# Kernel tuning notes

Hardware: AMD Instinct MI355X
Metric: run time of the kernel (lower is better)

The kernel has to match this reference:

```python
import jax, jax.numpy as jnp
import numpy as np

B, S, D = 1024, 200, 128
NQ, NC, NQD, NCD = 50000, 1000, 101, 101


def _linear_params(k, fan_in, fan_out):
    bound = 1.0 / np.sqrt(fan_in)
    kw, kb = jax.random.split(k)
    W = jax.random.uniform(kw, (fan_out, fan_in), minval=-bound, maxval=bound, dtype=jnp.float32)
    b = jax.random.uniform(kb, (fan_out,), minval=-bound, maxval=bound, dtype=jnp.float32)
    return W, b


def setup_inputs() -> dict:
    key = jax.random.key(0)
    ks = jax.random.split(key, 17)
    Wx, bx = _linear_params(ks[0], 4 * D, D)
    Ws1, bs1 = _linear_params(ks[1], D, D)
    Ws2, bs2 = _linear_params(ks[2], D, D)
    Wp1, bp1 = _linear_params(ks[3], 2 * D, D)
    Wp2, bp2 = _linear_params(ks[4], 2 * D, D)
    Wk, bk = _linear_params(ks[5], 4 * D, D)
    Eq = jax.random.normal(ks[6], (NQ, D), dtype=jnp.float32)
    Ec = jax.random.normal(ks[7], (NC, D), dtype=jnp.float32)
    Eqd = jax.random.normal(ks[8], (NQD, D), dtype=jnp.float32)
    Ecd = jax.random.normal(ks[9], (NCD, D), dtype=jnp.float32)
    Ecorr = jax.random.normal(ks[10], (2, D), dtype=jnp.float32)
    # xavier_uniform init for h_pre (torch: gain*sqrt(6/(fan_in+fan_out)) on [B,D])
    bh = np.sqrt(6.0 / (B + D))
    h0 = jax.random.uniform(ks[11], (B, D), minval=-bh, maxval=bh, dtype=jnp.float32)
    question_seq = jax.random.randint(ks[12], (B, S), 0, NQ)
    concept_seq = jax.random.randint(ks[13], (B, S), 0, NC)
    question_diff_seq = jax.random.randint(ks[14], (B, S), 0, NQD)
    concept_diff_seq = jax.random.randint(ks[15], (B, S), 0, NCD)
    correct_seq = jax.random.randint(ks[16], (B, S), 0, 2)
    return dict(question_seq=question_seq, concept_seq=concept_seq,
                question_diff_seq=question_diff_seq, concept_diff_seq=concept_diff_seq,
                correct_seq=correct_seq,
                Eq=Eq, Ec=Ec, Eqd=Eqd, Ecd=Ecd, Ecorr=Ecorr,
                Wx=Wx, bx=bx, Ws1=Ws1, bs1=bs1, Ws2=Ws2, bs2=bs2,
                Wp1=Wp1, bp1=bp1, Wp2=Wp2, bp2=bp2, Wk=Wk, bk=bk, h0=h0)


def reference(question_seq, concept_seq, question_diff_seq, concept_diff_seq, correct_seq,
              Eq, Ec, Eqd, Ecd, Ecorr,
              Wx, bx, Ws1, bs1, Ws2, bs2, Wp1, bp1, Wp2, bp2, Wk, bk, h0):
    qe = Eq[question_seq]            # [B,S,D]
    ce = Ec[concept_seq]
    qde = Eqd[question_diff_seq]
    cde = Ecd[concept_diff_seq]
    corr = Ecorr[correct_seq]
    # generate_x_MLP applied to all timesteps at once (same math as per-step)
    x = jnp.concatenate([qe, ce, qde, cde], axis=-1) @ Wx.T + bx  # [B,S,D]
    # time-major inputs for the scan over t = 0 .. S-2
    xs = (jnp.swapaxes(x[:, :-1], 0, 1),      # x_t       [S-1,B,D]
          jnp.swapaxes(x[:, 1:], 0, 1),       # x_{t+1}
          jnp.swapaxes(corr[:, :-1], 0, 1),
          jnp.swapaxes(qde[:, :-1], 0, 1),
          jnp.swapaxes(cde[:, :-1], 0, 1))

    def step(h_pre, inp):
        xt, xnext, ct, qdt, cdt = inp
        s_in = xt - h_pre
        sdf = jax.nn.sigmoid(s_in @ Ws1.T + bs1) * jnp.tanh(s_in @ Ws2.T + bs2)  # dropout=eval identity
        p_in = jnp.concatenate([sdf, ct], axis=-1)
        pka = jax.nn.sigmoid(p_in @ Wp1.T + bp1) * jnp.tanh(p_in @ Wp2.T + bp2)
        k_in = jnp.concatenate([h_pre, ct, qdt, cdt], axis=-1)
        g = jax.nn.sigmoid(k_in @ Wk.T + bk)
        h = g * h_pre + (1.0 - g) * pka
        yt = jax.nn.sigmoid(jnp.sum(xnext * h, axis=-1))  # [B]
        return h, yt

    _, ys = jax.lax.scan(step, h0, xs)  # ys: [S-1,B]
    y = jnp.concatenate([ys.T, jnp.zeros((question_seq.shape[0], 1), x.dtype)], axis=1)  # [B,S], y[:, S-1]=0
    return y
```

## Files before the change

### kernel.cpp

```cpp
#include <hip/hip_runtime.h>
#include <hip/hip_bf16.h>


#define S_LEN 200
#define NBATCH 1024
#define DIM 128
#define LOG2E 1.4426950408889634f

typedef short short8 __attribute__((ext_vector_type(8)));
typedef float f32x4 __attribute__((ext_vector_type(4)));

__device__ __forceinline__ unsigned short f2b(float f) {
  union { float f; unsigned u; } v; v.f = f;
  unsigned r = (v.u + 0x7FFFu + ((v.u >> 16) & 1u)) >> 16;
  return (unsigned short)r;
}
__device__ __forceinline__ float b2f(unsigned short b) {
  union { unsigned u; float f; } v; v.u = ((unsigned)b) << 16;
  return v.f;
}
__device__ __forceinline__ unsigned pk_bf16(float lo, float hi) {
  __hip_bfloat162 t = __float22bfloat162_rn(make_float2(lo, hi));
  union { __hip_bfloat162 h; unsigned u; } cv; cv.h = t;
  return cv.u;
}
__device__ __forceinline__ float fast_sigmoid(float x) {
  return __builtin_amdgcn_rcpf(1.0f + __builtin_amdgcn_exp2f(-LOG2E * x));
}
__device__ __forceinline__ float fast_tanh(float x) {
  return 2.0f * __builtin_amdgcn_rcpf(1.0f + __builtin_amdgcn_exp2f(-2.0f * LOG2E * x)) - 1.0f;
}
__device__ __forceinline__ void wg_barrier_lds() {
  __asm__ volatile("s_waitcnt lgkmcnt(0)\n\ts_barrier" ::: "memory");
}

__global__ void proj_all_kernel(const float* __restrict__ Eq, const float* __restrict__ Ec,
                                const float* __restrict__ Eqd, const float* __restrict__ Ecd,
                                const float* __restrict__ Ecorr,
                                const float* __restrict__ Wx,
                                const float* __restrict__ Wp1, const float* __restrict__ bp1,
                                const float* __restrict__ Wp2, const float* __restrict__ bp2,
                                const float* __restrict__ Wk, const float* __restrict__ bk,
                                unsigned short* __restrict__ Tq, unsigned short* __restrict__ Tc,
                                unsigned short* __restrict__ Tqd, unsigned short* __restrict__ Tcd,
                                unsigned short* __restrict__ Tkqd, unsigned short* __restrict__ Tkcd,
                                float* __restrict__ Tkc, float* __restrict__ Tp1c,
                                float* __restrict__ Tp2c) {
  const int bid = blockIdx.x;
  const int tid = threadIdx.x;
  if (bid >= 802) {
    const int blk = bid - 802;
    if (blk < 101) {
      const int o = tid & 127, half = tid >> 7;
      const float* e = (half ? Ecd : Eqd) + (size_t)blk * DIM;
      const float* wr = Wk + (size_t)o * 512 + (half ? 384 : 256);
      float a = 0.f;
      for (int k = 0; k < DIM; ++k) a = fmaf(e[k], wr[k], a);
      (half ? Tkcd : Tkqd)[blk * DIM + o] = f2b(a);
    } else {
      for (int idx = tid; idx < 768; idx += 256) {
        const int t = idx >> 8, e = (idx >> 7) & 1, o = idx & 127;
        const float* ec = Ecorr + e * DIM;
        const float* wr; float bias; float* dst;
        if (t == 0)      { wr = Wp1 + (size_t)o * 256 + 128; bias = bp1[o]; dst = Tp1c; }
        else if (t == 1) { wr = Wp2 + (size_t)o * 256 + 128; bias = bp2[o]; dst = Tp2c; }
        else             { wr = Wk  + (size_t)o * 512 + 128; bias = bk[o];  dst = Tkc;  }
        float a = bias;
        for (int k = 0; k < DIM; ++k) a = fmaf(ec[k], wr[k], a);
        dst[e * DIM + o] = a;
      }
    }
    return;
  }
  const float* E; int M, coff, r0; unsigned short* T;
  if (bid < 782)      { E = Eq;  M = 50000; coff = 0;   T = Tq;  r0 = bid * 64; }
  else if (bid < 798) { E = Ec;  M = 1000;  coff = 128; T = Tc;  r0 = (bid - 782) * 64; }
  else if (bid < 800) { E = Eqd; M = 101;   coff = 256; T = Tqd; r0 = (bid - 798) * 64; }
  else                { E = Ecd; M = 101;   coff = 384; T = Tcd; r0 = (bid - 800) * 64; }

  __shared__ __align__(16) unsigned short A[64][136];
  {
    const int row = tid >> 2, cb = (tid & 3) * 32;
    union U8 { uint4 v; unsigned short s[8]; } o;
#pragma unroll
    for (int cc = 0; cc < 4; ++cc) {
      const int c8 = cb + cc * 8;
      if (r0 + row < M) {
        const float4 e0 = *(const float4*)(E + (size_t)(r0 + row) * DIM + c8);
        const float4 e1 = *(const float4*)(E + (size_t)(r0 + row) * DIM + c8 + 4);
        o.s[0] = f2b(e0.x); o.s[1] = f2b(e0.y); o.s[2] = f2b(e0.z); o.s[3] = f2b(e0.w);
        o.s[4] = f2b(e1.x); o.s[5] = f2b(e1.y); o.s[6] = f2b(e1.z); o.s[7] = f2b(e1.w);
      } else {
        o.v = make_uint4(0, 0, 0, 0);
      }
      *(uint4*)&A[row][c8] = o.v;
    }
  }
  __syncthreads();
  const int w = tid >> 6, L = tid & 63, q = L >> 4, m = L & 15;
  short8 bf[2][4];
#pragma unroll
  for (int T2 = 0; T2 < 2; ++T2) {
    const int n = 32 * w + 16 * T2 + m;
#pragma unroll
    for (int kb = 0; kb < 4; ++kb) {
      const float* src = Wx + (size_t)n * 512 + coff + kb * 32 + q * 8;
      const float4 v0 = *(const float4*)src;
      const float4 v1 = *(const float4*)(src + 4);
      short8 f;
      f[0] = (short)f2b(v0.x); f[1] = (short)f2b(v0.y);
      f[2] = (short)f2b(v0.z); f[3] = (short)f2b(v0.w);
      f[4] = (short)f2b(v1.x); f[5] = (short)f2b(v1.y);
      f[6] = (short)f2b(v1.z); f[7] = (short)f2b(v1.w);
      bf[T2][kb] = f;
    }
  }
  const f32x4 vzero = {0.f, 0.f, 0.f, 0.f};
#pragma unroll
  for (int mt = 0; mt < 4; ++mt) {
    short8 af[4];
#pragma unroll
    for (int kb = 0; kb < 4; ++kb) af[kb] = *(const short8*)&A[mt * 16 + m][kb * 32 + q * 8];
    f32x4 acc[2] = {vzero, vzero};
#pragma unroll
    for (int kb = 0; kb < 4; ++kb) {
#pragma unroll
      for (int T2 = 0; T2 < 2; ++T2)
        acc[T2] = __builtin_amdgcn_mfma_f32_16x16x32_bf16(af[kb], bf[T2][kb], acc[T2], 0, 0, 0);
    }
#pragma unroll
    for (int T2 = 0; T2 < 2; ++T2) {
      const int col = 32 * w + 16 * T2 + m;
#pragma unroll
      for (int i = 0; i < 4; ++i) {
        const int r = r0 + mt * 16 + q * 4 + i;
        if (r < M) T[(size_t)r * DIM + col] = f2b(acc[T2][i]);
      }
    }
  }
}

__global__ void build_x_kernel(const int* __restrict__ qs, const int* __restrict__ cs,
                               const int* __restrict__ qds, const int* __restrict__ cds,
                               const int* __restrict__ corr,
                               const unsigned short* __restrict__ Tq, const unsigned short* __restrict__ Tc,
                               const unsigned short* __restrict__ Tqd, const unsigned short* __restrict__ Tcd,
                               const float* __restrict__ bx, unsigned short* __restrict__ xg,
                               float* __restrict__ SSg, float* __restrict__ corrf) {
  const int r = blockIdx.x * 16 + (threadIdx.x >> 4);
  const int c8 = (threadIdx.x & 15) * 8;
  const int s = r >> 10, b = r & 1023;
  const int q = qs[b * S_LEN + s], c = cs[b * S_LEN + s];
  const int qd = qds[b * S_LEN + s], cd = cds[b * S_LEN + s];
  union U8 { uint4 v; unsigned short s[8]; };
  U8 vq, vc, vd, ve, o;
  vq.v = *(const uint4*)(Tq + (size_t)q * DIM + c8);
  vc.v = *(const uint4*)(Tc + (size_t)c * DIM + c8);
  vd.v = *(const uint4*)(Tqd + (size_t)qd * DIM + c8);
  ve.v = *(const uint4*)(Tcd + (size_t)cd * DIM + c8);
  const float4 bx0 = *(const float4*)(bx + c8);
  const float4 bx1 = *(const float4*)(bx + c8 + 4);
  float bb[8] = {bx0.x, bx0.y, bx0.z, bx0.w, bx1.x, bx1.y, bx1.z, bx1.w};
  float part = 0.f;
#pragma unroll
  for (int j = 0; j < 8; ++j) {
    const float sv = b2f(vq.s[j]) + b2f(vc.s[j]) + b2f(vd.s[j]) + b2f(ve.s[j]) + bb[j];
    o.s[j] = f2b(sv);
    const float xr = b2f(o.s[j]);
    part = fmaf(xr, xr, part);
  }
  *(uint4*)(xg + (size_t)r * DIM + c8) = o.v;
#pragma unroll
  for (int off = 1; off <= 8; off <<= 1) part += __shfl_xor(part, off, 64);
  if ((threadIdx.x & 15) == 0) {
    SSg[r] = part;
    corrf[r] = (float)corr[b * S_LEN + s];
  }
}

__global__ void gemm_xg_kernel(const unsigned short* __restrict__ xg,
                               const float* __restrict__ Wk,
                               const int* __restrict__ corr, const int* __restrict__ qds,
                               const int* __restrict__ cds,
                               const float* __restrict__ Tkc,
                               const unsigned short* __restrict__ Tkqd,
                               const unsigned short* __restrict__ Tkcd,
                               unsigned short* __restrict__ GG) {
  const int tid = threadIdx.x;
  const int r0 = blockIdx.x * 64;
  __shared__ __align__(16) unsigned short TS[64][136];
  {
    const int row = tid >> 2, cb = (tid & 3) * 32;
    const int r = r0 + row, t = r >> 10, b = r & 1023;
    const int ci = corr[b * S_LEN + t], qi = qds[b * S_LEN + t], di = cds[b * S_LEN + t];
    union U8 { uint4 v; unsigned short s[8]; };
#pragma unroll
    for (int cc = 0; cc < 4; ++cc) {
      const int c8 = cb + cc * 8;
      U8 vq, vc, o;
      vq.v = *(const uint4*)(Tkqd + (size_t)qi * DIM + c8);
      vc.v = *(const uint4*)(Tkcd + (size_t)di * DIM + c8);
      const float4 k0 = *(const float4*)(Tkc + (size_t)ci * DIM + c8);
      const float4 k1 = *(const float4*)(Tkc + (size_t)ci * DIM + c8 + 4);
      float kk[8] = {k0.x, k0.y, k0.z, k0.w, k1.x, k1.y, k1.z, k1.w};
#pragma unroll
      for (int j = 0; j < 8; ++j) o.s[j] = f2b(kk[j] + b2f(vq.s[j]) + b2f(vc.s[j]));
      *(uint4*)&TS[row][c8] = o.v;
    }
  }
  __syncthreads();
  const int w = tid >> 6, L = tid & 63, q = L >> 4, m = L & 15;
  short8 wk[2][4];
#pragma unroll
  for (int T = 0; T < 2; ++T) {
    const int n = 32 * w + 16 * T + m;
#pragma unroll
    for (int kb = 0; kb < 4; ++kb) {
      const float* src = Wk + (size_t)n * 512 + kb * 32 + q * 8;
      const float4 v0 = *(const float4*)src;
      const float4 v1 = *(const float4*)(src + 4);
      short8 f;
      f[0] = (short)f2b(v0.x); f[1] = (short)f2b(v0.y);
      f[2] = (short)f2b(v0.z); f[3] = (short)f2b(v0.w);
      f[4] = (short)f2b(v1.x); f[5] = (short)f2b(v1.y);
      f[6] = (short)f2b(v1.z); f[7] = (short)f2b(v1.w);
      wk[T][kb] = f;
    }
  }
  const f32x4 vzero = {0.f, 0.f, 0.f, 0.f};
#pragma unroll
  for (int mt = 0; mt < 4; ++mt) {
    short8 af[4];
#pragma unroll
    for (int kb = 0; kb < 4; ++kb)
      af[kb] = *(const short8*)(xg + (size_t)(r0 + mt * 16 + m) * DIM + kb * 32 + q * 8);
    f32x4 acc[2] = {vzero, vzero};
#pragma unroll
    for (int kb = 0; kb < 4; ++kb) {
#pragma unroll
      for (int T = 0; T < 2; ++T)
        acc[T] = __builtin_amdgcn_mfma_f32_16x16x32_bf16(af[kb], wk[T][kb], acc[T], 0, 0, 0);
    }
#pragma unroll
    for (int T = 0; T < 2; ++T) {
      const int col = 32 * w + 16 * T + m;
#pragma unroll
      for (int i = 0; i < 4; ++i) {
        const int row64 = mt * 16 + q * 4 + i;
        GG[(size_t)(r0 + row64) * DIM + col] = f2b(acc[T][i] + b2f(TS[row64][col]));
      }
    }
  }
}

__global__ __launch_bounds__(512, 2) void scan_kernel(
    const unsigned short* __restrict__ xg,
    const unsigned short* __restrict__ gg,
    const float* __restrict__ SSg,
    const float* __restrict__ corrf,
    const float* __restrict__ h0,
    const float* __restrict__ Ws1, const float* __restrict__ bs1,
    const float* __restrict__ Ws2, const float* __restrict__ bs2,
    const float* __restrict__ Wp1, const float* __restrict__ Wp2,
    const float* __restrict__ Wk,
    const float* __restrict__ gTp1c, const float* __restrict__ gTp2c,
    float* __restrict__ outp) {
  __shared__ __align__(16) unsigned short Sbuf[16][136];
  __shared__ __align__(16) unsigned short Pbuf[16][136];

  const int tid = threadIdx.x;
  const int w = tid >> 6, L = tid & 63, q = L >> 4, m = L & 15;
  const int col16 = 16 * w + m;
  const int rbase = blockIdx.x << 4;
  const size_t SB = (size_t)NBATCH * DIM;

  short8 wf[5][4];
  {
    const float* Wptr[5] = {Ws1, Ws2, Wp1, Wp2, Wk};
    const int ldw[5] = {128, 128, 256, 256, 512};
#pragma unroll
    for (int M = 0; M < 5; ++M) {
#pragma unroll
      for (int kb = 0; kb < 4; ++kb) {
        const float* src = Wptr[M] + (size_t)col16 * ldw[M] + kb * 32 + q * 8;
        const float4 v0 = *(const float4*)src;
        const float4 v1 = *(const float4*)(src + 4);
        short8 f;
        f[0] = (short)f2b(v0.x); f[1] = (short)f2b(v0.y);
        f[2] = (short)f2b(v0.z); f[3] = (short)f2b(v0.w);
        f[4] = (short)f2b(v1.x); f[5] = (short)f2b(v1.y);
        f[6] = (short)f2b(v1.z); f[7] = (short)f2b(v1.w);
        wf[M][kb] = f;
      }
    }
  }
  const float bs1v = bs1[col16], bs2v = bs2[col16];
  const float tp1v0 = gTp1c[col16], dtp1 = gTp1c[DIM + col16] - tp1v0;
  const float tp2v0 = gTp2c[col16], dtp2 = gTp2c[DIM + col16] - tp2v0;

  float h[4];
#pragma unroll
  for (int i = 0; i < 4; ++i) {
    const int b = rbase + q * 4 + i;
    const float hv = h0[(size_t)b * DIM + col16];
    h[i] = hv;
    const float xt = b2f(xg[(size_t)b * DIM + col16]);
    Sbuf[q * 4 + i][col16] = f2b(xt - hv);
  }
  if (tid < 16) outp[(size_t)(rbase + tid) * S_LEN + (S_LEN - 1)] = 0.0f;
  float* poy = outp + (size_t)(rbase + m) * S_LEN;

  unsigned short XPA[4], XPB[4], GPA[4], GPB[4];
  float4 CFA, CFB;
  short8 XFA[4], XFB[4];
  float SSA, SSB;
  const unsigned short* pxA = xg + 3 * SB + (size_t)(rbase + q * 4) * DIM + col16;
  const unsigned short* pxB = pxA + SB;
  const unsigned short* pgA = gg + 2 * SB + (size_t)(rbase + q * 4) * DIM + col16;
  const unsigned short* pgB = pgA + SB;
  const float* pcA = corrf + 2 * NBATCH + rbase + q * 4;
  const float* pcB = pcA + NBATCH;
  const unsigned short* pfA = xg + 2 * SB + (size_t)(rbase + m) * DIM + q * 8;
  const unsigned short* pfB = pfA + SB;
  const float* psA = SSg + 2 * NBATCH + rbase + m;
  const float* psB = psA + NBATCH;
#pragma unroll
  for (int i = 0; i < 4; ++i) {
    XPA[i] = xg[SB + (size_t)(rbase + q * 4 + i) * DIM + col16];
    XPB[i] = xg[2 * SB + (size_t)(rbase + q * 4 + i) * DIM + col16];
    GPA[i] = gg[(size_t)(rbase + q * 4 + i) * DIM + col16];
    GPB[i] = gg[SB + (size_t)(rbase + q * 4 + i) * DIM + col16];
  }
  CFA = *(const float4*)(corrf + rbase + q * 4);
  CFB = *(const float4*)(corrf + NBATCH + rbase + q * 4);
#pragma unroll
  for (int kb = 0; kb < 4; ++kb) {
    XFA[kb] = *(const short8*)(xg + (size_t)(rbase + m) * DIM + kb * 32 + q * 8);
    XFB[kb] = *(const short8*)(xg + SB + (size_t)(rbase + m) * DIM + kb * 32 + q * 8);
  }
  SSA = SSg[rbase + m];
  SSB = SSg[NBATCH + rbase + m];

  const f32x4 vzero = {0.f, 0.f, 0.f, 0.f};

#define STEP(TCUR, XP, GP, CF, PX, PG, PC, XF, SSR, PF, PS)                    \
  do {                                                                         \
    const int t_ = (TCUR);                                                     \
    float xnv[4], ggv[4], cfv[4];                                              \
    _Pragma("unroll") for (int i = 0; i < 4; ++i) {                            \
      xnv[i] = b2f(XP[i]); ggv[i] = b2f(GP[i]);                                \
    }                                                                          \
    cfv[0] = CF.x; cfv[1] = CF.y; cfv[2] = CF.z; cfv[3] = CF.w;                \
    short8 xfr[4]; float ssv = SSR;                                            \
    if (w == 0) {                                                              \
      _Pragma("unroll") for (int kb = 0; kb < 4; ++kb) xfr[kb] = XF[kb];       \
    }                                                                          \
    _Pragma("unroll") for (int i = 0; i < 4; ++i) {                            \
      XP[i] = PX[i * DIM]; GP[i] = PG[i * DIM];                                \
    }                                                                          \
    CF = *(const float4*)PC;                                                   \
    PX += 2 * SB; PG += 2 * SB; PC += 2 * NBATCH;                              \
    if (w == 0) {                                                              \
      _Pragma("unroll") for (int kb = 0; kb < 4; ++kb)                         \
        XF[kb] = *(const short8*)(PF + kb * 32);                               \
      SSR = *PS;                                                               \
      PF += 2 * SB; PS += 2 * NBATCH;                                          \
    }                                                                          \
    wg_barrier_lds();                                       \
    short8 sf[4];                                                              \
    _Pragma("unroll") for (int kb = 0; kb < 4; ++kb)                           \
        sf[kb] = *(const short8*)&Sbuf[m][kb * 32 + q * 8];                    \
    f32x4 a1 = vzero, a2 = vzero, c1 = vzero;                                  \
    _Pragma("unroll") for (int kb = 0; kb < 4; ++kb) {                         \
      a1 = __builtin_amdgcn_mfma_f32_16x16x32_bf16(sf[kb], wf[0][kb], a1, 0, 0, 0); \
      a2 = __builtin_amdgcn_mfma_f32_16x16x32_bf16(sf[kb], wf[1][kb], a2, 0, 0, 0); \
      c1 = __builtin_amdgcn_mfma_f32_16x16x32_bf16(sf[kb], wf[4][kb], c1, 0, 0, 0); \
    }                                                                          \
    if (w == 0) {                                                              \
      f32x4 dt = vzero;                                                        \
      _Pragma("unroll") for (int kb = 0; kb < 4; ++kb)                         \
        dt = __builtin_amdgcn_mfma_f32_16x16x32_bf16(sf[kb], xfr[kb], dt, 0, 0, 0); \
      if (t_ > 0 && q == (m >> 2)) {                                           \
        const int ii = m & 3;                                                  \
        const float D = ii == 0 ? dt[0] : ii == 1 ? dt[1] : ii == 2 ? dt[2] : dt[3]; \
        poy[t_ - 1] = fast_sigmoid(ssv - D);                                   \
      }                                                                        \
    }                                                                          \
    _Pragma("unroll") for (int i2 = 0; i2 < 2; ++i2) {                         \
      const float s0 = fast_sigmoid(a1[2 * i2] + bs1v) * fast_tanh(a2[2 * i2] + bs2v); \
      const float s1 = fast_sigmoid(a1[2 * i2 + 1] + bs1v) * fast_tanh(a2[2 * i2 + 1] + bs2v); \
      const unsigned u = pk_bf16(s0, s1);                                      \
      Pbuf[q * 4 + 2 * i2][col16] = (unsigned short)u;                         \
      Pbuf[q * 4 + 2 * i2 + 1][col16] = (unsigned short)(u >> 16);             \
    }                                                                          \
    wg_barrier_lds();                                          \
    short8 pf[4];                                                              \
    _Pragma("unroll") for (int kb = 0; kb < 4; ++kb)                           \
        pf[kb] = *(const short8*)&Pbuf[m][kb * 32 + q * 8];                    \
    f32x4 p1 = vzero, p2 = vzero;                                              \
    _Pragma("unroll") for (int kb = 0; kb < 4; ++kb) {                         \
      p1 = __builtin_amdgcn_mfma_f32_16x16x32_bf16(pf[kb], wf[2][kb], p1, 0, 0, 0); \
      p2 = __builtin_amdgcn_mfma_f32_16x16x32_bf16(pf[kb], wf[3][kb], p2, 0, 0, 0); \
    }                                                                          \
    float sn[4];                                                               \
    _Pragma("unroll") for (int i = 0; i < 4; ++i) {                            \
      const float g = fast_sigmoid(ggv[i] - c1[i]);                            \
      const float t1v = fmaf(cfv[i], dtp1, tp1v0);                             \
      const float t2v = fmaf(cfv[i], dtp2, tp2v0);                             \
      const float pka = fast_sigmoid(p1[i] + t1v) * fast_tanh(p2[i] + t2v);    \
      const float hn = pka + g * (h[i] - pka);                                 \
      h[i] = hn;                                                               \
      sn[i] = xnv[i] - hn;                                                     \
    }                                                                          \
    _Pragma("unroll") for (int i2 = 0; i2 < 2; ++i2) {                         \
      const unsigned u = pk_bf16(sn[2 * i2], sn[2 * i2 + 1]);                  \
      Sbuf[q * 4 + 2 * i2][col16] = (unsigned short)u;                         \
      Sbuf[q * 4 + 2 * i2 + 1][col16] = (unsigned short)(u >> 16);             \
    }                                                                          \
  } while (0)

  for (int t2 = 0; t2 < 198; t2 += 2) {
    STEP(t2, XPA, GPA, CFA, pxA, pgA, pcA, XFA, SSA, pfA, psA);
    STEP(t2 + 1, XPB, GPB, CFB, pxB, pgB, pcB, XFB, SSB, pfB, psB);
  }
  STEP(198, XPA, GPA, CFA, pxA, pgA, pcA, XFA, SSA, pfA, psA);
#undef STEP

  wg_barrier_lds();
  if (w == 0) {
    short8 sf[4];
#pragma unroll
    for (int kb = 0; kb < 4; ++kb) sf[kb] = *(const short8*)&Sbuf[m][kb * 32 + q * 8];
    f32x4 dt = vzero;
#pragma unroll
    for (int kb = 0; kb < 4; ++kb)
      dt = __builtin_amdgcn_mfma_f32_16x16x32_bf16(sf[kb], XFB[kb], dt, 0, 0, 0);
    if (q == (m >> 2)) {
      const int ii = m & 3;
      const float D = ii == 0 ? dt[0] : ii == 1 ? dt[1] : ii == 2 ? dt[2] : dt[3];
      poy[S_LEN - 2] = fast_sigmoid(SSB - D);
    }
  }
}

extern "C" void kernel_launch(void* const* d_in, const int* in_sizes, int n_in,
                              void* d_out, int out_size, void* d_ws, size_t ws_size,
                              hipStream_t stream) {
  const int* qs    = (const int*)d_in[0];
  const int* cs    = (const int*)d_in[1];
  const int* qds   = (const int*)d_in[2];
  const int* cds   = (const int*)d_in[3];
  const int* corr  = (const int*)d_in[4];
  const float* Eq    = (const float*)d_in[5];
  const float* Ec    = (const float*)d_in[6];
  const float* Eqd   = (const float*)d_in[7];
  const float* Ecd   = (const float*)d_in[8];
  const float* Ecorr = (const float*)d_in[9];
  const float* Wx  = (const float*)d_in[10];
  const float* bx  = (const float*)d_in[11];
  const float* Ws1 = (const float*)d_in[12];
  const float* bs1 = (const float*)d_in[13];
  const float* Ws2 = (const float*)d_in[14];
  const float* bs2 = (const float*)d_in[15];
  const float* Wp1 = (const float*)d_in[16];
  const float* bp1 = (const float*)d_in[17];
  const float* Wp2 = (const float*)d_in[18];
  const float* bp2 = (const float*)d_in[19];
  const float* Wk  = (const float*)d_in[20];
  const float* bk  = (const float*)d_in[21];
  const float* h0  = (const float*)d_in[22];

  char* ws = (char*)d_ws;
  const size_t xbytes = (size_t)S_LEN * NBATCH * DIM * 2;
  const size_t A = (xbytes + 255) & ~(size_t)255;
  const size_t ggbytes = (size_t)(S_LEN - 1) * NBATCH * DIM * 2;
  unsigned short* X  = (unsigned short*)ws;
  unsigned short* GG = (unsigned short*)(ws + A);
  unsigned short* Tq  = GG;
  unsigned short* Tc  = (unsigned short*)(ws + A + (size_t)50000 * DIM * 2);
  unsigned short* Tqd = (unsigned short*)(ws + A + (size_t)51000 * DIM * 2);
  unsigned short* Tcd = (unsigned short*)(ws + A + (size_t)51101 * DIM * 2);
  size_t off = A + ((ggbytes + 255) & ~(size_t)255);
  auto alloc = [&](size_t bytes) {
    void* p = ws + off;
    off = (off + bytes + 255) & ~(size_t)255;
    return p;
  };
  float* corrf = (float*)alloc((size_t)S_LEN * NBATCH * 4);
  float* SS    = (float*)alloc((size_t)S_LEN * NBATCH * 4);
  unsigned short* Tkqd = (unsigned short*)alloc((size_t)101 * DIM * 2);
  unsigned short* Tkcd = (unsigned short*)alloc((size_t)101 * DIM * 2);
  float* Tkc  = (float*)alloc((size_t)2 * DIM * 4);
  float* Tp1c = (float*)alloc((size_t)2 * DIM * 4);
  float* Tp2c = (float*)alloc((size_t)2 * DIM * 4);

  proj_all_kernel<<<904, 256, 0, stream>>>(Eq, Ec, Eqd, Ecd, Ecorr, Wx,
                                           Wp1, bp1, Wp2, bp2, Wk, bk,
                                           Tq, Tc, Tqd, Tcd, Tkqd, Tkcd, Tkc, Tp1c, Tp2c);
  build_x_kernel<<<(S_LEN * NBATCH) / 16, 256, 0, stream>>>(qs, cs, qds, cds, corr,
                                                            Tq, Tc, Tqd, Tcd, bx, X, SS, corrf);
  gemm_xg_kernel<<<((S_LEN - 1) * NBATCH) / 64, 256, 0, stream>>>(X, Wk, corr, qds, cds,
                                                                  Tkc, Tkqd, Tkcd, GG);
  scan_kernel<<<64, 512, 0, stream>>>(X, GG, SS, corrf, h0, Ws1, bs1, Ws2, bs2,
                                      Wp1, Wp2, Wk, Tp1c, Tp2c, (float*)d_out);
}
```

Measured before the change: 515.5 us.

## Fuse input build and gate GEMM into scan kernel as producer blocks with watermark sync

Replaces the separate build_x and gemm_xg launches with a single persistent kernel. In it, 64 blocks run the recurrent scan while 191 producer blocks build X, SS, corr and the gate pre-activations per timestep chunk. A coordinator block turns per-timestep completion counters into a watermark that scan blocks poll before each step pair, so input production overlaps the serial scan. It relies on all 256 blocks being co-resident and adds atomic polling overhead. It also gives the workspace a non-aliased layout, falling back to the old path if the workspace is too small.

```diff
diff --git a/kernel.cpp b/kernel.cpp
--- a/kernel.cpp
+++ b/kernel.cpp
@@ -6,6 +6,7 @@
 #define NBATCH 1024
 #define DIM 128
 #define LOG2E 1.4426950408889634f
+#define NPROD 191
 
 typedef short short8 __attribute__((ext_vector_type(8)));
 typedef float f32x4 __attribute__((ext_vector_type(4)));
@@ -45,7 +46,7 @@
                                 unsigned short* __restrict__ Tqd, unsigned short* __restrict__ Tcd,
                                 unsigned short* __restrict__ Tkqd, unsigned short* __restrict__ Tkcd,
                                 float* __restrict__ Tkc, float* __restrict__ Tp1c,
-                                float* __restrict__ Tp2c) {
+                                float* __restrict__ Tp2c, int* __restrict__ syncz) {
   const int bid = blockIdx.x;
   const int tid = threadIdx.x;
   if (bid >= 802) {
@@ -69,6 +70,7 @@
         for (int k = 0; k < DIM; ++k) a = fmaf(ec[k], wr[k], a);
         dst[e * DIM + o] = a;
       }
+      for (int i2 = tid; i2 < 272; i2 += 256) syncz[i2] = 0;
     }
     return;
   }
@@ -253,20 +255,129 @@
   }
 }
 
-__global__ __launch_bounds__(512, 2) void scan_kernel(
-    const unsigned short* __restrict__ xg,
-    const unsigned short* __restrict__ gg,
-    const float* __restrict__ SSg,
-    const float* __restrict__ corrf,
+__device__ __forceinline__ void producer_body(
+    const int p,
+    const int* __restrict__ qs, const int* __restrict__ cs,
+    const int* __restrict__ qds, const int* __restrict__ cds,
+    const int* __restrict__ corr,
+    const unsigned short* __restrict__ Tq, const unsigned short* __restrict__ Tc,
+    const unsigned short* __restrict__ Tqd, const unsigned short* __restrict__ Tcd,
+    const float* __restrict__ bx, const float* __restrict__ Wk,
+    const float* __restrict__ Tkc, const unsigned short* __restrict__ Tkqd,
+    const unsigned short* __restrict__ Tkcd,
+    unsigned short* __restrict__ X, unsigned short* __restrict__ GG,
+    float* __restrict__ SSg, float* __restrict__ corrf,
+    int* donecnt, unsigned short (*xtile)[136], unsigned short (*TS)[136]) {
+  const int tid = threadIdx.x;
+  const int w = tid >> 6, L = tid & 63, q = L >> 4, m = L & 15;
+  const int n = 16 * w + m;
+  short8 wk[4];
+#pragma unroll
+  for (int kb = 0; kb < 4; ++kb) {
+    const float* src = Wk + (size_t)n * 512 + kb * 32 + q * 8;
+    const float4 v0 = *(const float4*)src;
+    const float4 v1 = *(const float4*)(src + 4);
+    short8 f;
+    f[0] = (short)f2b(v0.x); f[1] = (short)f2b(v0.y);
+    f[2] = (short)f2b(v0.z); f[3] = (short)f2b(v0.w);
+    f[4] = (short)f2b(v1.x); f[5] = (short)f2b(v1.y);
+    f[6] = (short)f2b(v1.z); f[7] = (short)f2b(v1.w);
+    wk[kb] = f;
+  }
+  const int row = tid >> 3, k8 = tid & 7;
+  const int c0 = k8 * 16;
+  float bxv[16];
+#pragma unroll
+  for (int j = 0; j < 4; ++j) {
+    const float4 bv = *(const float4*)(bx + c0 + j * 4);
+    bxv[4 * j + 0] = bv.x; bxv[4 * j + 1] = bv.y;
+    bxv[4 * j + 2] = bv.z; bxv[4 * j + 3] = bv.w;
+  }
+  const f32x4 vzero = {0.f, 0.f, 0.f, 0.f};
+  union U8 { uint4 v; unsigned short s[8]; };
+
+  for (int i = p; i < 3200; i += NPROD) {
+    const int t = i >> 4, c = i & 15;
+    const int b = c * 64 + row;
+    const int base = b * S_LEN + t;
+    const int qi = qs[base], ci = cs[base], qdi = qds[base], cdi = cds[base], cri = corr[base];
+    float part = 0.f;
+#pragma unroll
+    for (int jj = 0; jj < 2; ++jj) {
+      const int c8 = c0 + jj * 8;
+      U8 vq, vc, vd, ve, o;
+      vq.v = *(const uint4*)(Tq + (size_t)qi * DIM + c8);
+      vc.v = *(const uint4*)(Tc + (size_t)ci * DIM + c8);
+      vd.v = *(const uint4*)(Tqd + (size_t)qdi * DIM + c8);
+      ve.v = *(const uint4*)(Tcd + (size_t)cdi * DIM + c8);
+#pragma unroll
+      for (int j = 0; j < 8; ++j) {
+        const float sv = b2f(vq.s[j]) + b2f(vc.s[j]) + b2f(vd.s[j]) + b2f(ve.s[j]) + bxv[jj * 8 + j];
+        o.s[j] = f2b(sv);
+        const float xr = b2f(o.s[j]);
+        part = fmaf(xr, xr, part);
+      }
+      *(uint4*)&xtile[row][c8] = o.v;
+      *(uint4*)(X + (size_t)(t * 1024 + b) * DIM + c8) = o.v;
+    }
+#pragma unroll
+    for (int off2 = 1; off2 <= 4; off2 <<= 1) part += __shfl_xor(part, off2, 64);
+    if (k8 == 0) {
+      SSg[t * 1024 + b] = part;
+      corrf[t * 1024 + b] = (float)cri;
+    }
+    if (t < 199) {
+#pragma unroll
+      for (int jj = 0; jj < 2; ++jj) {
+        const int c8 = c0 + jj * 8;
+        U8 vq, vc, o;
+        vq.v = *(const uint4*)(Tkqd + (size_t)qdi * DIM + c8);
+        vc.v = *(const uint4*)(Tkcd + (size_t)cdi * DIM + c8);
+        const float4 k0 = *(const float4*)(Tkc + (size_t)cri * DIM + c8);
+        const float4 k1 = *(const float4*)(Tkc + (size_t)cri * DIM + c8 + 4);
+        float kk[8] = {k0.x, k0.y, k0.z, k0.w, k1.x, k1.y, k1.z, k1.w};
+#pragma unroll
+        for (int j = 0; j < 8; ++j) o.s[j] = f2b(kk[j] + b2f(vq.s[j]) + b2f(vc.s[j]));
+        *(uint4*)&TS[row][c8] = o.v;
+      }
+    }
+    __syncthreads();
+    if (t < 199) {
+#pragma unroll
+      for (int mt = 0; mt < 4; ++mt) {
+        short8 af[4];
+#pragma unroll
+        for (int kb = 0; kb < 4; ++kb) af[kb] = *(const short8*)&xtile[mt * 16 + m][kb * 32 + q * 8];
+        f32x4 acc = vzero;
+#pragma unroll
+        for (int kb = 0; kb < 4; ++kb)
+          acc = __builtin_amdgcn_mfma_f32_16x16x32_bf16(af[kb], wk[kb], acc, 0, 0, 0);
+#pragma unroll
+        for (int i2 = 0; i2 < 4; ++i2) {
+          const int row64 = mt * 16 + q * 4 + i2;
+          GG[(size_t)(t * 1024 + c * 64 + row64) * DIM + n] = f2b(acc[i2] + b2f(TS[row64][n]));
+        }
+      }
+    }
+    __syncthreads();
+    if (tid == 0)
+      __hip_atomic_fetch_add(donecnt + t, 1, __ATOMIC_RELEASE, __HIP_MEMORY_SCOPE_AGENT);
+  }
+}
+
+template <bool PIPE>
+__device__ __forceinline__ void scan_body(
+    const unsigned short* __restrict__ xg, const unsigned short* __restrict__ gg,
+    const float* __restrict__ SSg, const float* __restrict__ corrf,
     const float* __restrict__ h0,
     const float* __restrict__ Ws1, const float* __restrict__ bs1,
     const float* __restrict__ Ws2, const float* __restrict__ bs2,
     const float* __restrict__ Wp1, const float* __restrict__ Wp2,
     const float* __restrict__ Wk,
     const float* __restrict__ gTp1c, const float* __restrict__ gTp2c,
-    float* __restrict__ outp) {
-  __shared__ __align__(16) unsigned short Sbuf[16][136];
-  __shared__ __align__(16) unsigned short Pbuf[16][136];
+    float* __restrict__ outp, int* wmp, unsigned short* ldsbase) {
+  unsigned short (*Sbuf)[136] = (unsigned short (*)[136])ldsbase;
+  unsigned short (*Pbuf)[136] = (unsigned short (*)[136])(ldsbase + 16 * 136);
 
   const int tid = threadIdx.x;
   const int w = tid >> 6, L = tid & 63, q = L >> 4, m = L & 15;
@@ -297,6 +408,16 @@
   const float bs1v = bs1[col16], bs2v = bs2[col16];
   const float tp1v0 = gTp1c[col16], dtp1 = gTp1c[DIM + col16] - tp1v0;
   const float tp2v0 = gTp2c[col16], dtp2 = gTp2c[DIM + col16] - tp2v0;
+  if (tid < 16) outp[(size_t)(rbase + tid) * S_LEN + (S_LEN - 1)] = 0.0f;
+
+  int wm_seen = 0;
+  auto wait_wm = [&](int need) {
+    if (wm_seen >= need) return;
+    while (__hip_atomic_load(wmp, __ATOMIC_RELAXED, __HIP_MEMORY_SCOPE_AGENT) < need)
+      __builtin_amdgcn_s_sleep(8);
+    wm_seen = __hip_atomic_load(wmp, __ATOMIC_ACQUIRE, __HIP_MEMORY_SCOPE_AGENT);
+  };
+  if (PIPE) wait_wm(3);
 
   float h[4];
 #pragma unroll
@@ -307,7 +428,6 @@
     const float xt = b2f(xg[(size_t)b * DIM + col16]);
     Sbuf[q * 4 + i][col16] = f2b(xt - hv);
   }
-  if (tid < 16) outp[(size_t)(rbase + tid) * S_LEN + (S_LEN - 1)] = 0.0f;
   float* poy = outp + (size_t)(rbase + m) * S_LEN;
 
   unsigned short XPA[4], XPB[4], GPA[4], GPB[4];
@@ -420,6 +540,10 @@
   } while (0)
 
   for (int t2 = 0; t2 < 198; t2 += 2) {
+    if (PIPE) {
+      const int need = (t2 + 5 > 200) ? 200 : t2 + 5;
+      wait_wm(need);
+    }
     STEP(t2, XPA, GPA, CFA, pxA, pgA, pcA, XFA, SSA, pfA, psA);
     STEP(t2 + 1, XPB, GPB, CFB, pxB, pgB, pcB, XFB, SSB, pfB, psB);
   }
@@ -440,6 +564,52 @@
       const float D = ii == 0 ? dt[0] : ii == 1 ? dt[1] : ii == 2 ? dt[2] : dt[3];
       poy[S_LEN - 2] = fast_sigmoid(SSB - D);
     }
+  }
+}
+
+template <bool PIPE>
+__global__ __launch_bounds__(512, 2) void scan_fused_kernel(
+    const unsigned short* __restrict__ xg, const unsigned short* __restrict__ gg,
+    const float* __restrict__ SSg, const float* __restrict__ corrf,
+    const float* __restrict__ h0,
+    const float* __restrict__ Ws1, const float* __restrict__ bs1,
+    const float* __restrict__ Ws2, const float* __restrict__ bs2,
+    const float* __restrict__ Wp1, const float* __restrict__ Wp2,
+    const float* __restrict__ WkF,
+    const float* __restrict__ gTp1c, const float* __restrict__ gTp2c,
+    float* __restrict__ outp,
+    const int* __restrict__ qs, const int* __restrict__ cs,
+    const int* __restrict__ qds, const int* __restrict__ cds,
+    const int* __restrict__ corr,
+    const unsigned short* __restrict__ Tq, const unsigned short* __restrict__ Tc,
+    const unsigned short* __restrict__ Tqd, const unsigned short* __restrict__ Tcd,
+    const float* __restrict__ bx, const float* __restrict__ Tkc,
+    const unsigned short* __restrict__ Tkqd, const unsigned short* __restrict__ Tkcd,
+    unsigned short* __restrict__ Xw, unsigned short* __restrict__ GGw,
+    float* __restrict__ SSw, float* __restrict__ corrw,
+    int* donecnt, int* wmp) {
+  __shared__ __align__(16) unsigned short lds[PIPE ? 2 * 64 * 136 : 2 * 16 * 136];
+  if (!PIPE || blockIdx.x < 64) {
+    scan_body<PIPE>(xg, gg, SSg, corrf, h0, Ws1, bs1, Ws2, bs2, Wp1, Wp2, WkF,
+                    gTp1c, gTp2c, outp, wmp, lds);
+    return;
+  }
+  if constexpr (PIPE) {
+    if (blockIdx.x == 255) {
+      if (threadIdx.x == 0) {
+        for (int t = 0; t < S_LEN; ++t) {
+          while (__hip_atomic_load(donecnt + t, __ATOMIC_RELAXED, __HIP_MEMORY_SCOPE_AGENT) < 16)
+            __builtin_amdgcn_s_sleep(8);
+          (void)__hip_atomic_load(donecnt + t, __ATOMIC_ACQUIRE, __HIP_MEMORY_SCOPE_AGENT);
+          __hip_atomic_store(wmp, t + 1, __ATOMIC_RELEASE, __HIP_MEMORY_SCOPE_AGENT);
+        }
+      }
+      return;
+    }
+    producer_body(blockIdx.x - 64, qs, cs, qds, cds, corr, Tq, Tc, Tqd, Tcd, bx,
+                  WkF, Tkc, Tkqd, Tkcd, Xw, GGw, SSw, corrw, donecnt,
+                  (unsigned short (*)[136])lds,
+                  (unsigned short (*)[136])(lds + 64 * 136));
   }
 }
 
@@ -472,8 +642,43 @@
 
   char* ws = (char*)d_ws;
   const size_t xbytes = (size_t)S_LEN * NBATCH * DIM * 2;
+  const size_t ggbytes = (size_t)(S_LEN - 1) * NBATCH * DIM * 2;
+
+  {
+    size_t off = 0;
+    auto alloc = [&](size_t bytes) {
+      void* p = ws + off;
+      off = (off + bytes + 255) & ~(size_t)255;
+      return p;
+    };
+    unsigned short* X  = (unsigned short*)alloc(xbytes);
+    unsigned short* GG = (unsigned short*)alloc(ggbytes);
+    float* corrf = (float*)alloc((size_t)S_LEN * NBATCH * 4);
+    float* SS    = (float*)alloc((size_t)S_LEN * NBATCH * 4);
+    unsigned short* Tq  = (unsigned short*)alloc((size_t)50000 * DIM * 2);
+    unsigned short* Tc  = (unsigned short*)alloc((size_t)1000 * DIM * 2);
+    unsigned short* Tqd = (unsigned short*)alloc((size_t)101 * DIM * 2);
+    unsigned short* Tcd = (unsigned short*)alloc((size_t)101 * DIM * 2);
+    unsigned short* Tkqd = (unsigned short*)alloc((size_t)101 * DIM * 2);
+    unsigned short* Tkcd = (unsigned short*)alloc((size_t)101 * DIM * 2);
+    float* Tkc  = (float*)alloc((size_t)2 * DIM * 4);
+    float* Tp1c = (float*)alloc((size_t)2 * DIM * 4);
+    float* Tp2c = (float*)alloc((size_t)2 * DIM * 4);
+    int* syncz  = (int*)alloc(2048);
+    if (off <= ws_size) {
+      proj_all_kernel<<<904, 256, 0, stream>>>(Eq, Ec, Eqd, Ecd, Ecorr, Wx,
+                                               Wp1, bp1, Wp2, bp2, Wk, bk,
+                                               Tq, Tc, Tqd, Tcd, Tkqd, Tkcd,
+                                               Tkc, Tp1c, Tp2c, syncz);
+      scan_fused_kernel<true><<<256, 512, 0, stream>>>(
+          X, GG, SS, corrf, h0, Ws1, bs1, Ws2, bs2, Wp1, Wp2, Wk, Tp1c, Tp2c,
+          (float*)d_out, qs, cs, qds, cds, corr, Tq, Tc, Tqd, Tcd, bx,
+          Tkc, Tkqd, Tkcd, X, GG, SS, corrf, syncz, syncz + 256);
+      return;
+    }
+  }
+
   const size_t A = (xbytes + 255) & ~(size_t)255;
-  const size_t ggbytes = (size_t)(S_LEN - 1) * NBATCH * DIM * 2;
   unsigned short* X  = (unsigned short*)ws;
   unsigned short* GG = (unsigned short*)(ws + A);
   unsigned short* Tq  = GG;
@@ -493,14 +698,18 @@
   float* Tkc  = (float*)alloc((size_t)2 * DIM * 4);
   float* Tp1c = (float*)alloc((size_t)2 * DIM * 4);
   float* Tp2c = (float*)alloc((size_t)2 * DIM * 4);
+  int* syncz  = (int*)alloc(2048);
 
   proj_all_kernel<<<904, 256, 0, stream>>>(Eq, Ec, Eqd, Ecd, Ecorr, Wx,
                                            Wp1, bp1, Wp2, bp2, Wk, bk,
-                                           Tq, Tc, Tqd, Tcd, Tkqd, Tkcd, Tkc, Tp1c, Tp2c);
+                                           Tq, Tc, Tqd, Tcd, Tkqd, Tkcd, Tkc, Tp1c, Tp2c,
+                                           syncz);
   build_x_kernel<<<(S_LEN * NBATCH) / 16, 256, 0, stream>>>(qs, cs, qds, cds, corr,
                                                             Tq, Tc, Tqd, Tcd, bx, X, SS, corrf);
   gemm_xg_kernel<<<((S_LEN - 1) * NBATCH) / 64, 256, 0, stream>>>(X, Wk, corr, qds, cds,
                                                                   Tkc, Tkqd, Tkcd, GG);
-  scan_kernel<<<64, 512, 0, stream>>>(X, GG, SS, corrf, h0, Ws1, bs1, Ws2, bs2,
-                                      Wp1, Wp2, Wk, Tp1c, Tp2c, (float*)d_out);
-}
+  scan_fused_kernel<false><<<64, 512, 0, stream>>>(
+      X, GG, SS, corrf, h0, Ws1, bs1, Ws2, bs2, Wp1, Wp2, Wk, Tp1c, Tp2c,
+      (float*)d_out, qs, cs, qds, cds, corr, Tq, Tc, Tqd, Tcd, bx,
+      Tkc, Tkqd, Tkcd, X, GG, SS, corrf, syncz, syncz + 256);
+}
```

After: 491.7 us. 1.05x faster.
